# Performance work log

Hardware: AMD Instinct MI355X
Metric: run time of the kernel (lower is better)

## Reference

```python
import jax, jax.numpy as jnp
import numpy as np

B, N, E = 64, 1024, 16384  # graphs, nodes per graph, edges per graph
N_ITER = 5
NORMALIZE = True
NUM_INIT_LABELS = 16


def _unique_inverse(h):
    """Equivalent of torch.unique(h, sorted=True, return_inverse=True)[1] for 1-D h."""
    order = jnp.argsort(h)
    sh = h[order]
    bnd = jnp.concatenate([jnp.zeros(1, jnp.int32), (sh[1:] != sh[:-1]).astype(jnp.int32)])
    ranks = jnp.cumsum(bnd)  # dense rank in sorted-unique order
    return jnp.zeros_like(ranks).at[order].set(ranks)


def _wl_iteration(mask, labels, hash_w):
    """One WL iteration for all graphs.
    mask: [B,N,N] bool dense adjacency (sparse-to-dense, as in the torch code)
    labels: [B,N] int32
    hash_w: [2] float32 (Linear(2,1,bias=False) weight)
    Returns new labels [B,N] int32.
    """
    w0, w1 = hash_w[0], hash_w[1]
    lab_f = labels.astype(jnp.float32)
    deg = mask.sum(-1).astype(jnp.float32)                      # [B,N] valid-neighbor count
    K = deg.max(axis=-1, keepdims=True)                         # per-graph max_neighbors
    # sum of neighbor labels (gather+reduce over the dense mask, memory-bound)
    seg = jnp.einsum('bij,bj->bi', mask.astype(jnp.float32), lab_f)  # [B,N]
    # torch builds [N,max_neighbors] rows: node label in col 0-feature, sorted
    # neighbor labels (padded with -1) in col 1-feature, hashes each pair with
    # w0*node + w1*neigh and sums over columns. Closed form (sort is sum-invariant):
    #   K*w0*node + w1*(sum_neighbors - (K - deg))
    hashed = K * w0 * lab_f + w1 * (seg + deg - K)              # [B,N]
    return jax.vmap(_unique_inverse)(hashed)


def setup_inputs() -> dict:
    key = jax.random.key(0)
    k1, k2, k3, k4 = jax.random.split(key, 4)
    edge_src = jax.random.randint(k1, (B, E), 0, N, dtype=jnp.int32)
    edge_dst = jax.random.randint(k2, (B, E), 0, N, dtype=jnp.int32)
    labels = jax.random.randint(k3, (B, N), 0, NUM_INIT_LABELS, dtype=jnp.int32)
    hash_w = jax.random.normal(k4, (2,), dtype=jnp.float32)
    return {"edge_src": edge_src, "edge_dst": edge_dst, "labels": labels, "hash_w": hash_w}


def reference(edge_src, edge_dst, labels, hash_w):
    # sparse-to-dense neighbor mask, as in the torch module
    b_idx = jnp.arange(B, dtype=jnp.int32)[:, None]
    mask = jnp.zeros((B, N, N), dtype=bool).at[b_idx, edge_src, edge_dst].set(True)

    all_labels = [labels]
    for _ in range(N_ITER):
        all_labels.append(_wl_iteration(mask, all_labels[-1], hash_w))

    # feature vectors: per graph, bincount of labels summed over all iterations.
    # Labels are always < N (unique-inverse ranks < N; initial labels < 16),
    # so N bins is a tight static upper bound for torch's max_label+1; the extra
    # zero columns do not change the Gram matrix.
    labels_all = jnp.stack(all_labels, axis=1).reshape(B, -1)   # [B, (n_iter+1)*N]
    feats = jax.vmap(lambda l: jnp.zeros((N,), jnp.float32).at[l].add(1.0))(labels_all)

    kernel = feats @ feats.T                                    # [B,B]
    if NORMALIZE:
        d = jnp.sqrt(jnp.diag(kernel))
        kernel = kernel / (d[None, :] * d[:, None])
    return kernel
```

## Files before the change

### kernel.cpp

```cpp
#include <hip/hip_runtime.h>

#define B 64
#define N 1024
#define E 16384
#define WPR 32
#define NITER 5
#define CSR_SLOTS (E + N)
#define MAXP 20
#define SENT_PAIR 0x04000400u
#define CAP 8
#define GSTRIDE 9

#define FEATS_OFF 0
#define DIAG_OFF  ((size_t)B * N * 4)

__global__ void __launch_bounds__(1024) wl_mega_k(const int* __restrict__ src,
                                                  const int* __restrict__ dstp,
                                                  const int* __restrict__ lab0,
                                                  const float* __restrict__ hw,
                                                  unsigned int* __restrict__ feats,
                                                  float* __restrict__ diag) {
    __shared__ union {
        unsigned int chunk[N * WPR];
        struct {
            unsigned short nbr[CSR_SLOTS];
            struct {
                int hist[N];
                int scan[N];
                float grp[N];
                int flag[N];
                float grp2[N * GSTRIDE];
            } pb;
        } s;
    } u;
    __shared__ int s_lab[N + 2];
    __shared__ unsigned int s_feats[N];
    __shared__ int s_wsum[16];
    __shared__ int s_kp[16];
    __shared__ float s_mn[16], s_mx[16];
    __shared__ int s_anytie;
    __shared__ int s_ovf;
    int b = blockIdx.x, t = threadIdx.x;
    int lane = t & 63, w = t >> 6;

    const int* sg = src + (size_t)b * E;
    const int* dg_ = dstp + (size_t)b * E;
    int es[16], ed[16];
#pragma unroll
    for (int k = 0; k < 16; ++k) {
        es[k] = sg[t + k * 1024];
        ed[k] = dg_[t + k * 1024];
    }
    int l0 = lab0[(size_t)b * N + t];
    float w0 = hw[0], w1 = hw[1];
#pragma unroll
    for (int k = 0; k < 8; ++k)
        ((uint4*)u.chunk)[t + k * 1024] = make_uint4(0, 0, 0, 0);
    s_lab[t] = l0;
    s_feats[t] = 0;
    if (t == 0) { s_lab[N] = 0; s_anytie = 0; s_ovf = 0; }
    __syncthreads();
#pragma unroll
    for (int v = 0; v < 16; ++v) {
        unsigned long long m = __ballot(l0 == v);
        if (lane == v) {
            int c = __popcll(m);
            if (c) atomicAdd(&s_feats[v], (unsigned)c);
        }
    }

#pragma unroll
    for (int k = 0; k < 16; ++k) {
        int wlog = ed[k] >> 5;
        int g = wlog >> 2;
        int p = (g + es[k]) & 7;
        atomicOr(&u.chunk[es[k] * WPR + p * 4 + (wlog & 3)], 1u << (ed[k] & 31));
    }
    __syncthreads();
    uint4 r[8];
    {
        const uint4* row4 = (const uint4*)(u.chunk + t * WPR);
#pragma unroll
        for (int g = 0; g < 8; ++g)
            r[g] = row4[(g + t) & 7];
    }
    __syncthreads();

    int dg = 0;
#pragma unroll
    for (int k = 0; k < 8; ++k)
        dg += __popc(r[k].x) + __popc(r[k].y) + __popc(r[k].z) + __popc(r[k].w);
    int alloc = (dg + 1) & ~1;

    int f = alloc;
#pragma unroll
    for (int d2 = 1; d2 < 64; d2 <<= 1) {
        int v = __shfl_up(f, d2);
        if (lane >= d2) f += v;
    }
    int km = dg;
#pragma unroll
    for (int o = 32; o > 0; o >>= 1) km = max(km, __shfl_down(km, o));
    if (lane == 63) s_wsum[w] = f;
    if (lane == 0)  s_kp[w] = km;
    __syncthreads();
    float Kf;
    int start;
    {
        int vv = ((lane & 15) < w) ? s_wsum[lane & 15] : 0;
#pragma unroll
        for (int m2 = 1; m2 < 16; m2 <<= 1) vv += __shfl_xor(vv, m2);
        start = (f - alloc) + vv;
        int kk = s_kp[lane & 15];
#pragma unroll
        for (int m2 = 8; m2 >= 1; m2 >>= 1) kk = max(kk, __shfl_xor(kk, m2));
        Kf = (float)kk;
    }
    u.s.pb.hist[t] = 0;
    u.s.pb.flag[t] = 0;

    {
        int idx = start;
#pragma unroll
        for (int k = 0; k < 8; ++k) {
            unsigned int wv[4] = { r[k].x, r[k].y, r[k].z, r[k].w };
#pragma unroll
            for (int c2 = 0; c2 < 4; ++c2) {
                unsigned int word = wv[c2];
                int bb = (k * 4 + c2) << 5;
                while (word) {
                    int j = __ffs(word) - 1;
                    word &= word - 1;
                    u.s.nbr[idx++] = (unsigned short)(bb + j);
                }
            }
        }
        if (dg & 1) u.s.nbr[idx] = (unsigned short)N;
    }
    asm volatile("" ::: "memory");

    int vdeg = dg;
    int vpstart = start >> 1;
    int vpairs = alloc >> 1;
    int lab_reg = l0;
    const unsigned int* nbr32 = (const unsigned int*)u.s.nbr;
    unsigned int pw[MAXP];
#pragma unroll
    for (int k = 0; k < MAXP; ++k)
        pw[k] = (k < vpairs) ? nbr32[vpstart + k] : SENT_PAIR;

    int nfast = 0;
    for (int it = 0; it < NITER; ++it) {
        int ssum = 0;
#pragma unroll
        for (int k = 0; k < MAXP; ++k) {
            unsigned int pr = pw[k];
            ssum += s_lab[pr & 0xFFFFu] + s_lab[pr >> 16];
        }
        for (int k = MAXP; k < vpairs; ++k) {
            unsigned int pr = nbr32[vpstart + k];
            ssum += s_lab[pr & 0xFFFFu] + s_lab[pr >> 16];
        }
        float t1 = __fmul_rn(__fmul_rn(Kf, w0), (float)lab_reg);
        float t2 = __fmul_rn(w1, __fsub_rn(__fadd_rn((float)ssum, (float)vdeg), Kf));
        float h  = __fadd_rn(t1, t2);

        float mn = h, mx = h;
#pragma unroll
        for (int o = 32; o > 0; o >>= 1) {
            mn = fminf(mn, __shfl_down(mn, o));
            mx = fmaxf(mx, __shfl_down(mx, o));
        }
        if (lane == 0) { s_mn[w] = mn; s_mx[w] = mx; }
        __syncthreads();
        float fmn, span;
        {
            float a = s_mn[lane & 15];
            float cmx = s_mx[lane & 15];
#pragma unroll
            for (int m2 = 8; m2 >= 1; m2 >>= 1) {
                a = fminf(a, __shfl_xor(a, m2));
                cmx = fmaxf(cmx, __shfl_xor(cmx, m2));
            }
            fmn = a;
            span = cmx - a;
        }
        float scale = (span > 0.f) ? (1023.0f / span) : 0.f;
        int bucket = min((int)((h - fmn) * scale), 1023);
        int off_in = atomicAdd(&u.s.pb.hist[bucket], 1);
        if (off_in < CAP) u.s.pb.grp2[bucket * GSTRIDE + off_in] = h;
        else s_ovf = 1;
        __syncthreads();

        int ovf = s_ovf;
        int cnt = u.s.pb.hist[bucket];
        int c_in = 0, eq = 0;
        if (!ovf) {
            for (int j = 0; j < cnt; ++j) {
                float g = u.s.pb.grp2[bucket * GSTRIDE + j];
                c_in += (g < h);
                eq += (g == h);
            }
        }
        f = u.s.pb.hist[t];
#pragma unroll
        for (int d2 = 1; d2 < 64; d2 <<= 1) {
            int v = __shfl_up(f, d2);
            if (lane >= d2) f += v;
        }
        if (lane == 63) s_wsum[w] = f;
        __syncthreads();
        {
            int vv = ((lane & 15) < w) ? s_wsum[lane & 15] : 0;
#pragma unroll
            for (int m2 = 1; m2 < 16; m2 <<= 1) vv += __shfl_xor(vv, m2);
            u.s.pb.scan[t] = f + vv;
        }
        u.s.pb.hist[t] = 0;
        if (t == 0) s_ovf = 0;
        __syncthreads();

        int cr;
        if (!ovf) {
            cr = (u.s.pb.scan[bucket] - cnt) + c_in;
        } else {
            int bs = u.s.pb.scan[bucket] - cnt;
            u.s.pb.grp[bs + off_in] = h;
            __syncthreads();
            cr = bs;
            eq = 0;
            for (int k = bs; k < bs + cnt; ++k) {
                float g = u.s.pb.grp[k];
                cr += (g < h);
                eq += (g == h);
            }
        }
        if (eq > 1) s_anytie = it + 1;
        s_lab[t] = cr;
        __syncthreads();
        if (s_anytie == it + 1) {
            u.s.pb.flag[cr] = 1;
            __syncthreads();
            int f2 = u.s.pb.flag[t];
#pragma unroll
            for (int d2 = 1; d2 < 64; d2 <<= 1) {
                int v = __shfl_up(f2, d2);
                if (lane >= d2) f2 += v;
            }
            if (lane == 63) s_wsum[w] = f2;
            __syncthreads();
            {
                int vv = ((lane & 15) < w) ? s_wsum[lane & 15] : 0;
#pragma unroll
                for (int m2 = 1; m2 < 16; m2 <<= 1) vv += __shfl_xor(vv, m2);
                u.s.pb.scan[t] = f2 + vv;
            }
            u.s.pb.flag[t] = 0;
            __syncthreads();
            int rank = u.s.pb.scan[cr] - 1;
            s_lab[t] = rank;
            lab_reg = rank;
            atomicAdd(&s_feats[rank], 1u);
            __syncthreads();
        } else {
            lab_reg = cr;
            ++nfast;
        }
    }

    unsigned int fv = s_feats[t] + (unsigned)nfast;
    feats[(size_t)b * N + t] = fv;
    int sq = (int)(fv * fv);
#pragma unroll
    for (int o = 32; o > 0; o >>= 1) sq += __shfl_down(sq, o);
    if (lane == 0) s_wsum[w] = sq;
    __syncthreads();
    if (t == 0) {
        int tot = 0;
#pragma unroll
        for (int k = 0; k < 16; ++k) tot += s_wsum[k];
        diag[b] = (float)tot;
    }
}

__global__ void __launch_bounds__(1024) gram_k(const unsigned int* __restrict__ feats,
                                               const float* __restrict__ diag,
                                               float* __restrict__ out) {
    __shared__ unsigned int s_fi[N];
    int i = blockIdx.x, t = threadIdx.x;
    int lane = t & 63, w = t >> 6;
    if (t < 256)
        ((uint4*)s_fi)[t] = ((const uint4*)(feats + (size_t)i * N))[t];
    __syncthreads();
    float di = diag[i];
#pragma unroll
    for (int jj = 0; jj < 4; ++jj) {
        int j = w * 4 + jj;
        const uint4* fj = (const uint4*)(feats + (size_t)j * N);
        const uint4* fi = (const uint4*)s_fi;
        int s = 0;
#pragma unroll
        for (int k = 0; k < 4; ++k) {
            uint4 vb = fj[lane + k * 64];
            uint4 va = fi[lane + k * 64];
            s += (int)(va.x * vb.x) + (int)(va.y * vb.y)
               + (int)(va.z * vb.z) + (int)(va.w * vb.w);
        }
#pragma unroll
        for (int off = 32; off > 0; off >>= 1) s += __shfl_down(s, off);
        if (lane == 0) out[i * B + j] = (float)s / sqrtf(di * diag[j]);
    }
}

extern "C" void kernel_launch(void* const* d_in, const int* in_sizes, int n_in,
                              void* d_out, int out_size, void* d_ws, size_t ws_size,
                              hipStream_t stream) {
    const int*   esrc = (const int*)d_in[0];
    const int*   edst = (const int*)d_in[1];
    const int*   lab0 = (const int*)d_in[2];
    const float* hw   = (const float*)d_in[3];

    char* ws = (char*)d_ws;
    unsigned int* feats = (unsigned int*)(ws + FEATS_OFF);
    float*        diag  = (float*)(ws + DIAG_OFF);

    wl_mega_k<<<B, 1024, 0, stream>>>(esrc, edst, lab0, hw, feats, diag);
    gram_k<<<B, 1024, 0, stream>>>(feats, diag, (float*)d_out);
}
```

Before: 98.28 us.

## Halve WL kernel block size to 512 threads, two nodes per thread

Reworks the WL mega-kernel so each of 512 threads handles two adjacent nodes instead of one node per thread across 1024 threads. Edge loading, bitmap building, CSR construction, neighbor-label sums, bucketed ranking and the scans are all duplicated per thread, and the cross-wave reductions shrink from 16 to 8 waves. The aim is cheaper barriers and reductions with more independent work per thread for latency hiding, at the cost of much higher register pressure (two 20-entry pair arrays plus 16 extra edge registers) and fewer resident waves per block.

New measurement: 101.1 us. +2.8%, slower.

```diff
diff --git a/kernel.cpp b/kernel.cpp
--- a/kernel.cpp
+++ b/kernel.cpp
@@ -10,16 +10,17 @@
 #define SENT_PAIR 0x04000400u
 #define CAP 8
 #define GSTRIDE 9
+#define NT 512
 
 #define FEATS_OFF 0
 #define DIAG_OFF  ((size_t)B * N * 4)
 
-__global__ void __launch_bounds__(1024) wl_mega_k(const int* __restrict__ src,
-                                                  const int* __restrict__ dstp,
-                                                  const int* __restrict__ lab0,
-                                                  const float* __restrict__ hw,
-                                                  unsigned int* __restrict__ feats,
-                                                  float* __restrict__ diag) {
+__global__ void __launch_bounds__(NT) wl_mega_k(const int* __restrict__ src,
+                                                const int* __restrict__ dstp,
+                                                const int* __restrict__ lab0,
+                                                const float* __restrict__ hw,
+                                                unsigned int* __restrict__ feats,
+                                                float* __restrict__ diag) {
     __shared__ union {
         unsigned int chunk[N * WPR];
         struct {
@@ -35,40 +36,48 @@
     } u;
     __shared__ int s_lab[N + 2];
     __shared__ unsigned int s_feats[N];
-    __shared__ int s_wsum[16];
-    __shared__ int s_kp[16];
-    __shared__ float s_mn[16], s_mx[16];
+    __shared__ int s_wsum[8];
+    __shared__ int s_kp[8];
+    __shared__ float s_mn[8], s_mx[8];
     __shared__ int s_anytie;
     __shared__ int s_ovf;
     int b = blockIdx.x, t = threadIdx.x;
     int lane = t & 63, w = t >> 6;
+    int n0 = t * 2, n1 = t * 2 + 1;
 
     const int* sg = src + (size_t)b * E;
     const int* dg_ = dstp + (size_t)b * E;
     int es[16], ed[16];
 #pragma unroll
     for (int k = 0; k < 16; ++k) {
-        es[k] = sg[t + k * 1024];
-        ed[k] = dg_[t + k * 1024];
-    }
-    int l0 = lab0[(size_t)b * N + t];
+        es[k] = sg[t + k * NT];
+        ed[k] = dg_[t + k * NT];
+    }
+    int2 l0p = *(const int2*)(lab0 + (size_t)b * N + n0);
     float w0 = hw[0], w1 = hw[1];
 #pragma unroll
-    for (int k = 0; k < 8; ++k)
-        ((uint4*)u.chunk)[t + k * 1024] = make_uint4(0, 0, 0, 0);
-    s_lab[t] = l0;
-    s_feats[t] = 0;
+    for (int k = 0; k < 16; ++k)
+        ((uint4*)u.chunk)[t + k * NT] = make_uint4(0, 0, 0, 0);
+    *(int2*)&s_lab[n0] = l0p;
+    ((uint2*)s_feats)[t] = make_uint2(0u, 0u);
     if (t == 0) { s_lab[N] = 0; s_anytie = 0; s_ovf = 0; }
     __syncthreads();
 #pragma unroll
     for (int v = 0; v < 16; ++v) {
-        unsigned long long m = __ballot(l0 == v);
+        unsigned long long m0 = __ballot(l0p.x == v);
+        unsigned long long m1 = __ballot(l0p.y == v);
         if (lane == v) {
-            int c = __popcll(m);
+            int c = __popcll(m0) + __popcll(m1);
             if (c) atomicAdd(&s_feats[v], (unsigned)c);
         }
     }
 
+    int es2[16], ed2[16];
+#pragma unroll
+    for (int k = 0; k < 16; ++k) {
+        es2[k] = sg[8192 + t + k * NT];
+        ed2[k] = dg_[8192 + t + k * NT];
+    }
 #pragma unroll
     for (int k = 0; k < 16; ++k) {
         int wlog = ed[k] >> 5;
@@ -76,54 +85,66 @@
         int p = (g + es[k]) & 7;
         atomicOr(&u.chunk[es[k] * WPR + p * 4 + (wlog & 3)], 1u << (ed[k] & 31));
     }
-    __syncthreads();
-    uint4 r[8];
+#pragma unroll
+    for (int k = 0; k < 16; ++k) {
+        int wlog = ed2[k] >> 5;
+        int g = wlog >> 2;
+        int p = (g + es2[k]) & 7;
+        atomicOr(&u.chunk[es2[k] * WPR + p * 4 + (wlog & 3)], 1u << (ed2[k] & 31));
+    }
+    __syncthreads();
+    uint4 r0[8], r1[8];
     {
-        const uint4* row4 = (const uint4*)(u.chunk + t * WPR);
-#pragma unroll
-        for (int g = 0; g < 8; ++g)
-            r[g] = row4[(g + t) & 7];
-    }
-    __syncthreads();
-
-    int dg = 0;
-#pragma unroll
-    for (int k = 0; k < 8; ++k)
-        dg += __popc(r[k].x) + __popc(r[k].y) + __popc(r[k].z) + __popc(r[k].w);
-    int alloc = (dg + 1) & ~1;
-
-    int f = alloc;
+        const uint4* rowA = (const uint4*)(u.chunk + n0 * WPR);
+        const uint4* rowB = (const uint4*)(u.chunk + n1 * WPR);
+#pragma unroll
+        for (int g = 0; g < 8; ++g) r0[g] = rowA[(g + n0) & 7];
+#pragma unroll
+        for (int g = 0; g < 8; ++g) r1[g] = rowB[(g + n1) & 7];
+    }
+    __syncthreads();
+
+    int dg0 = 0, dg1 = 0;
+#pragma unroll
+    for (int k = 0; k < 8; ++k) {
+        dg0 += __popc(r0[k].x) + __popc(r0[k].y) + __popc(r0[k].z) + __popc(r0[k].w);
+        dg1 += __popc(r1[k].x) + __popc(r1[k].y) + __popc(r1[k].z) + __popc(r1[k].w);
+    }
+    int alloc0 = (dg0 + 1) & ~1, alloc1 = (dg1 + 1) & ~1;
+    int ps = alloc0 + alloc1;
+    int f = ps;
 #pragma unroll
     for (int d2 = 1; d2 < 64; d2 <<= 1) {
         int v = __shfl_up(f, d2);
         if (lane >= d2) f += v;
     }
-    int km = dg;
+    int km = max(dg0, dg1);
 #pragma unroll
     for (int o = 32; o > 0; o >>= 1) km = max(km, __shfl_down(km, o));
     if (lane == 63) s_wsum[w] = f;
     if (lane == 0)  s_kp[w] = km;
     __syncthreads();
     float Kf;
-    int start;
+    int start0, start1;
     {
-        int vv = ((lane & 15) < w) ? s_wsum[lane & 15] : 0;
-#pragma unroll
-        for (int m2 = 1; m2 < 16; m2 <<= 1) vv += __shfl_xor(vv, m2);
-        start = (f - alloc) + vv;
-        int kk = s_kp[lane & 15];
-#pragma unroll
-        for (int m2 = 8; m2 >= 1; m2 >>= 1) kk = max(kk, __shfl_xor(kk, m2));
+        int vv = ((lane & 7) < w) ? s_wsum[lane & 7] : 0;
+#pragma unroll
+        for (int m2 = 1; m2 < 8; m2 <<= 1) vv += __shfl_xor(vv, m2);
+        start0 = (f - ps) + vv;
+        start1 = start0 + alloc0;
+        int kk = s_kp[lane & 7];
+#pragma unroll
+        for (int m2 = 4; m2 >= 1; m2 >>= 1) kk = max(kk, __shfl_xor(kk, m2));
         Kf = (float)kk;
     }
-    u.s.pb.hist[t] = 0;
-    u.s.pb.flag[t] = 0;
+    ((int2*)u.s.pb.hist)[t] = make_int2(0, 0);
+    ((int2*)u.s.pb.flag)[t] = make_int2(0, 0);
 
     {
-        int idx = start;
+        int idx = start0;
 #pragma unroll
         for (int k = 0; k < 8; ++k) {
-            unsigned int wv[4] = { r[k].x, r[k].y, r[k].z, r[k].w };
+            unsigned int wv[4] = { r0[k].x, r0[k].y, r0[k].z, r0[k].w };
 #pragma unroll
             for (int c2 = 0; c2 < 4; ++c2) {
                 unsigned int word = wv[c2];
@@ -135,37 +156,60 @@
                 }
             }
         }
-        if (dg & 1) u.s.nbr[idx] = (unsigned short)N;
+        if (dg0 & 1) u.s.nbr[idx] = (unsigned short)N;
+        idx = start1;
+#pragma unroll
+        for (int k = 0; k < 8; ++k) {
+            unsigned int wv[4] = { r1[k].x, r1[k].y, r1[k].z, r1[k].w };
+#pragma unroll
+            for (int c2 = 0; c2 < 4; ++c2) {
+                unsigned int word = wv[c2];
+                int bb = (k * 4 + c2) << 5;
+                while (word) {
+                    int j = __ffs(word) - 1;
+                    word &= word - 1;
+                    u.s.nbr[idx++] = (unsigned short)(bb + j);
+                }
+            }
+        }
+        if (dg1 & 1) u.s.nbr[idx] = (unsigned short)N;
     }
     asm volatile("" ::: "memory");
 
-    int vdeg = dg;
-    int vpstart = start >> 1;
-    int vpairs = alloc >> 1;
-    int lab_reg = l0;
+    int vpairs0 = alloc0 >> 1, vpairs1 = alloc1 >> 1;
+    int vps0 = start0 >> 1, vps1 = start1 >> 1;
+    int lr0 = l0p.x, lr1 = l0p.y;
     const unsigned int* nbr32 = (const unsigned int*)u.s.nbr;
-    unsigned int pw[MAXP];
-#pragma unroll
-    for (int k = 0; k < MAXP; ++k)
-        pw[k] = (k < vpairs) ? nbr32[vpstart + k] : SENT_PAIR;
+    unsigned int pw0[MAXP], pw1[MAXP];
+#pragma unroll
+    for (int k = 0; k < MAXP; ++k) {
+        pw0[k] = (k < vpairs0) ? nbr32[vps0 + k] : SENT_PAIR;
+        pw1[k] = (k < vpairs1) ? nbr32[vps1 + k] : SENT_PAIR;
+    }
 
     int nfast = 0;
     for (int it = 0; it < NITER; ++it) {
-        int ssum = 0;
+        int ss0 = 0, ss1 = 0;
 #pragma unroll
         for (int k = 0; k < MAXP; ++k) {
-            unsigned int pr = pw[k];
-            ssum += s_lab[pr & 0xFFFFu] + s_lab[pr >> 16];
-        }
-        for (int k = MAXP; k < vpairs; ++k) {
-            unsigned int pr = nbr32[vpstart + k];
-            ssum += s_lab[pr & 0xFFFFu] + s_lab[pr >> 16];
-        }
-        float t1 = __fmul_rn(__fmul_rn(Kf, w0), (float)lab_reg);
-        float t2 = __fmul_rn(w1, __fsub_rn(__fadd_rn((float)ssum, (float)vdeg), Kf));
-        float h  = __fadd_rn(t1, t2);
-
-        float mn = h, mx = h;
+            unsigned int pa = pw0[k], pb2 = pw1[k];
+            ss0 += s_lab[pa & 0xFFFFu] + s_lab[pa >> 16];
+            ss1 += s_lab[pb2 & 0xFFFFu] + s_lab[pb2 >> 16];
+        }
+        for (int k = MAXP; k < vpairs0; ++k) {
+            unsigned int pr = nbr32[vps0 + k];
+            ss0 += s_lab[pr & 0xFFFFu] + s_lab[pr >> 16];
+        }
+        for (int k = MAXP; k < vpairs1; ++k) {
+            unsigned int pr = nbr32[vps1 + k];
+            ss1 += s_lab[pr & 0xFFFFu] + s_lab[pr >> 16];
+        }
+        float h0 = __fadd_rn(__fmul_rn(__fmul_rn(Kf, w0), (float)lr0),
+                             __fmul_rn(w1, __fsub_rn(__fadd_rn((float)ss0, (float)dg0), Kf)));
+        float h1 = __fadd_rn(__fmul_rn(__fmul_rn(Kf, w0), (float)lr1),
+                             __fmul_rn(w1, __fsub_rn(__fadd_rn((float)ss1, (float)dg1), Kf)));
+
+        float mn = fminf(h0, h1), mx = fmaxf(h0, h1);
 #pragma unroll
         for (int o = 32; o > 0; o >>= 1) {
             mn = fminf(mn, __shfl_down(mn, o));
@@ -175,10 +219,10 @@
         __syncthreads();
         float fmn, span;
         {
-            float a = s_mn[lane & 15];
-            float cmx = s_mx[lane & 15];
-#pragma unroll
-            for (int m2 = 8; m2 >= 1; m2 >>= 1) {
+            float a = s_mn[lane & 7];
+            float cmx = s_mx[lane & 7];
+#pragma unroll
+            for (int m2 = 4; m2 >= 1; m2 >>= 1) {
                 a = fminf(a, __shfl_xor(a, m2));
                 cmx = fmaxf(cmx, __shfl_xor(cmx, m2));
             }
@@ -186,23 +230,35 @@
             span = cmx - a;
         }
         float scale = (span > 0.f) ? (1023.0f / span) : 0.f;
-        int bucket = min((int)((h - fmn) * scale), 1023);
-        int off_in = atomicAdd(&u.s.pb.hist[bucket], 1);
-        if (off_in < CAP) u.s.pb.grp2[bucket * GSTRIDE + off_in] = h;
+        int bk0 = min((int)((h0 - fmn) * scale), 1023);
+        int bk1 = min((int)((h1 - fmn) * scale), 1023);
+        int off0 = atomicAdd(&u.s.pb.hist[bk0], 1);
+        if (off0 < CAP) u.s.pb.grp2[bk0 * GSTRIDE + off0] = h0;
+        else s_ovf = 1;
+        int off1 = atomicAdd(&u.s.pb.hist[bk1], 1);
+        if (off1 < CAP) u.s.pb.grp2[bk1 * GSTRIDE + off1] = h1;
         else s_ovf = 1;
         __syncthreads();
 
         int ovf = s_ovf;
-        int cnt = u.s.pb.hist[bucket];
-        int c_in = 0, eq = 0;
+        int cnt0 = u.s.pb.hist[bk0];
+        int cnt1 = u.s.pb.hist[bk1];
+        int c0 = 0, eq0 = 0, c1 = 0, eq1 = 0;
         if (!ovf) {
-            for (int j = 0; j < cnt; ++j) {
-                float g = u.s.pb.grp2[bucket * GSTRIDE + j];
-                c_in += (g < h);
-                eq += (g == h);
-            }
-        }
-        f = u.s.pb.hist[t];
+            for (int j = 0; j < cnt0; ++j) {
+                float g = u.s.pb.grp2[bk0 * GSTRIDE + j];
+                c0 += (g < h0);
+                eq0 += (g == h0);
+            }
+            for (int j = 0; j < cnt1; ++j) {
+                float g = u.s.pb.grp2[bk1 * GSTRIDE + j];
+                c1 += (g < h1);
+                eq1 += (g == h1);
+            }
+        }
+        int2 hp = ((int2*)u.s.pb.hist)[t];
+        int hs = hp.x + hp.y;
+        f = hs;
 #pragma unroll
         for (int d2 = 1; d2 < 64; d2 <<= 1) {
             int v = __shfl_up(f, d2);
@@ -211,37 +267,50 @@
         if (lane == 63) s_wsum[w] = f;
         __syncthreads();
         {
-            int vv = ((lane & 15) < w) ? s_wsum[lane & 15] : 0;
-#pragma unroll
-            for (int m2 = 1; m2 < 16; m2 <<= 1) vv += __shfl_xor(vv, m2);
-            u.s.pb.scan[t] = f + vv;
-        }
-        u.s.pb.hist[t] = 0;
+            int vv = ((lane & 7) < w) ? s_wsum[lane & 7] : 0;
+#pragma unroll
+            for (int m2 = 1; m2 < 8; m2 <<= 1) vv += __shfl_xor(vv, m2);
+            u.s.pb.scan[n0] = vv + f - hs + hp.x;
+            u.s.pb.scan[n1] = vv + f;
+        }
+        ((int2*)u.s.pb.hist)[t] = make_int2(0, 0);
         if (t == 0) s_ovf = 0;
         __syncthreads();
 
-        int cr;
+        int cr0, cr1;
         if (!ovf) {
-            cr = (u.s.pb.scan[bucket] - cnt) + c_in;
+            cr0 = (u.s.pb.scan[bk0] - cnt0) + c0;
+            cr1 = (u.s.pb.scan[bk1] - cnt1) + c1;
         } else {
-            int bs = u.s.pb.scan[bucket] - cnt;
-            u.s.pb.grp[bs + off_in] = h;
+            int bs0 = u.s.pb.scan[bk0] - cnt0;
+            int bs1 = u.s.pb.scan[bk1] - cnt1;
+            u.s.pb.grp[bs0 + off0] = h0;
+            u.s.pb.grp[bs1 + off1] = h1;
             __syncthreads();
-            cr = bs;
-            eq = 0;
-            for (int k = bs; k < bs + cnt; ++k) {
+            cr0 = bs0; eq0 = 0;
+            for (int k = bs0; k < bs0 + cnt0; ++k) {
                 float g = u.s.pb.grp[k];
-                cr += (g < h);
-                eq += (g == h);
-            }
-        }
-        if (eq > 1) s_anytie = it + 1;
-        s_lab[t] = cr;
+                cr0 += (g < h0);
+                eq0 += (g == h0);
+            }
+            cr1 = bs1; eq1 = 0;
+            for (int k = bs1; k < bs1 + cnt1; ++k) {
+                float g = u.s.pb.grp[k];
+                cr1 += (g < h1);
+                eq1 += (g == h1);
+            }
+        }
+        if ((eq0 > 1) || (eq1 > 1)) s_anytie = it + 1;
+        s_lab[n0] = cr0;
+        s_lab[n1] = cr1;
         __syncthreads();
         if (s_anytie == it + 1) {
-            u.s.pb.flag[cr] = 1;
+            u.s.pb.flag[cr0] = 1;
+            u.s.pb.flag[cr1] = 1;
             __syncthreads();
-            int f2 = u.s.pb.flag[t];
+            int2 fp = ((int2*)u.s.pb.flag)[t];
+            int fs = fp.x + fp.y;
+            int f2 = fs;
 #pragma unroll
             for (int d2 = 1; d2 < 64; d2 <<= 1) {
                 int v = __shfl_up(f2, d2);
@@ -250,27 +319,34 @@
             if (lane == 63) s_wsum[w] = f2;
             __syncthreads();
             {
-                int vv = ((lane & 15) < w) ? s_wsum[lane & 15] : 0;
-#pragma unroll
-                for (int m2 = 1; m2 < 16; m2 <<= 1) vv += __shfl_xor(vv, m2);
-                u.s.pb.scan[t] = f2 + vv;
-            }
-            u.s.pb.flag[t] = 0;
+                int vv = ((lane & 7) < w) ? s_wsum[lane & 7] : 0;
+#pragma unroll
+                for (int m2 = 1; m2 < 8; m2 <<= 1) vv += __shfl_xor(vv, m2);
+                u.s.pb.scan[n0] = vv + f2 - fs + fp.x;
+                u.s.pb.scan[n1] = vv + f2;
+            }
+            ((int2*)u.s.pb.flag)[t] = make_int2(0, 0);
             __syncthreads();
-            int rank = u.s.pb.scan[cr] - 1;
-            s_lab[t] = rank;
-            lab_reg = rank;
-            atomicAdd(&s_feats[rank], 1u);
+            int rank0 = u.s.pb.scan[cr0] - 1;
+            int rank1 = u.s.pb.scan[cr1] - 1;
+            s_lab[n0] = rank0;
+            s_lab[n1] = rank1;
+            lr0 = rank0;
+            lr1 = rank1;
+            atomicAdd(&s_feats[rank0], 1u);
+            atomicAdd(&s_feats[rank1], 1u);
             __syncthreads();
         } else {
-            lab_reg = cr;
+            lr0 = cr0;
+            lr1 = cr1;
             ++nfast;
         }
     }
 
-    unsigned int fv = s_feats[t] + (unsigned)nfast;
-    feats[(size_t)b * N + t] = fv;
-    int sq = (int)(fv * fv);
+    unsigned int fv0 = s_feats[n0] + (unsigned)nfast;
+    unsigned int fv1 = s_feats[n1] + (unsigned)nfast;
+    *(uint2*)(feats + (size_t)b * N + n0) = make_uint2(fv0, fv1);
+    int sq = (int)(fv0 * fv0 + fv1 * fv1);
 #pragma unroll
     for (int o = 32; o > 0; o >>= 1) sq += __shfl_down(sq, o);
     if (lane == 0) s_wsum[w] = sq;
@@ -278,7 +354,7 @@
     if (t == 0) {
         int tot = 0;
 #pragma unroll
-        for (int k = 0; k < 16; ++k) tot += s_wsum[k];
+        for (int k = 0; k < 8; ++k) tot += s_wsum[k];
         diag[b] = (float)tot;
     }
 }
@@ -324,6 +400,6 @@
     unsigned int* feats = (unsigned int*)(ws + FEATS_OFF);
     float*        diag  = (float*)(ws + DIAG_OFF);
 
-    wl_mega_k<<<B, 1024, 0, stream>>>(esrc, edst, lab0, hw, feats, diag);
+    wl_mega_k<<<B, NT, 0, stream>>>(esrc, edst, lab0, hw, feats, diag);
     gram_k<<<B, 1024, 0, stream>>>(feats, diag, (float*)d_out);
 }
```
